# Performance work log

Hardware: AMD Instinct MI355X
Metric: run time of the kernel (lower is better)

The kernel has to match this reference:

```python
import jax, jax.numpy as jnp
import numpy as np

B, S, E = 2, 2048, 2048
H, KVH = 16, 4
D = E // H            # 128
N_REP = H // KVH      # 4


def setup_inputs() -> dict:
    key = jax.random.key(0)
    ks = jax.random.split(key, 5)
    x = jax.random.normal(ks[0], (B, S, E), dtype=jnp.float32)
    # kaiming-normal-ish linear weights, torch layout [out_features, in_features]
    wq_w = jax.random.normal(ks[1], (H * D, E), dtype=jnp.float32) * (2.0 / E) ** 0.5
    wk_w = jax.random.normal(ks[2], (KVH * D, E), dtype=jnp.float32) * (2.0 / E) ** 0.5
    wv_w = jax.random.normal(ks[3], (KVH * D, E), dtype=jnp.float32) * (2.0 / E) ** 0.5
    wo_w = jax.random.normal(ks[4], (E, E), dtype=jnp.float32) * (2.0 / E) ** 0.5
    # standard RoPE frequencies: theta = 10000
    inv_freq = 1.0 / (10000.0 ** (np.arange(0, D, 2, dtype=np.float32) / D))  # [D/2]
    t = np.arange(S, dtype=np.float32)
    ang = np.outer(t, inv_freq)  # [S, D/2]
    freqs_cos = jnp.asarray(np.cos(ang), dtype=jnp.float32)
    freqs_sin = jnp.asarray(np.sin(ang), dtype=jnp.float32)
    return {"x": x, "wq_w": wq_w, "wk_w": wk_w, "wv_w": wv_w, "wo_w": wo_w,
            "freqs_cos": freqs_cos, "freqs_sin": freqs_sin, "start_pos": 0}


def _rope(t, cos, sin):
    # t: [B, S, h, D]; cos/sin: [S, D/2] -> complex multiply on (even, odd) pairs
    tr = t.reshape(*t.shape[:-1], -1, 2)
    xr, xi = tr[..., 0], tr[..., 1]
    c = cos[None, :, None, :]
    s = sin[None, :, None, :]
    orr = xr * c - xi * s
    oi = xr * s + xi * c
    return jnp.stack([orr, oi], axis=-1).reshape(t.shape)


def reference(x, wq_w, wk_w, wv_w, wo_w, freqs_cos, freqs_sin, start_pos):
    b, s, e = x.shape
    q = jnp.einsum('bse,fe->bsf', x, wq_w).reshape(b, s, H, D)
    k = jnp.einsum('bse,fe->bsf', x, wk_w).reshape(b, s, KVH, D)
    v = jnp.einsum('bse,fe->bsf', x, wv_w).reshape(b, s, KVH, D)
    q = _rope(q, freqs_cos, freqs_sin)
    k = _rope(k, freqs_cos, freqs_sin)
    # faithful to torch .repeat(1,1,n_rep,1): TILE kv heads -> head h uses kv head h % KVH
    k = jnp.tile(k, (1, 1, N_REP, 1))  # [b, s, H, D]
    v = jnp.tile(v, (1, 1, N_REP, 1))
    q = q.transpose(0, 2, 1, 3)  # [b, H, s, D]
    k = k.transpose(0, 2, 1, 3)
    v = v.transpose(0, 2, 1, 3)
    scores = jnp.einsum('bhqd,bhkd->bhqk', q, k) * (1.0 / D ** 0.5)
    causal = jnp.tril(jnp.ones((s, s), dtype=bool))
    scores = jnp.where(causal[None, None], scores, -jnp.inf)
    attn = jax.nn.softmax(scores, axis=-1)
    out = jnp.einsum('bhqk,bhkd->bhqd', attn, v)
    out = out.transpose(0, 2, 1, 3).reshape(b, s, e)
    return jnp.einsum('bse,fe->bsf', out, wo_w)
```

## Files before the change

### kernel.cpp

```cpp
#include <hip/hip_runtime.h>
#include <hip/hip_bf16.h>

typedef unsigned short u16;
typedef unsigned int u32;
typedef short bf16x8 __attribute__((ext_vector_type(8)));
typedef float f32x4 __attribute__((ext_vector_type(4)));

#define MFMA_BF16 __builtin_amdgcn_mfma_f32_16x16x32_bf16

#define B_   2
#define S_   2048
#define E_   2048
#define H_   16
#define KVH_ 4
#define D_   128
#define M_   (B_ * S_)
#define NQKV 3072
#define SCALE_ 0.08838834764831845f

__device__ __forceinline__ float b2f(u16 u) {
    union { u32 i; float f; } x; x.i = ((u32)u) << 16; return x.f;
}
__device__ __forceinline__ u16 f2b(float f) {
    __hip_bfloat16 h = __float2bfloat16(f);
    return *reinterpret_cast<u16*>(&h);
}

__device__ __forceinline__ void async16(const u16* g, u16* l) {
    __builtin_amdgcn_global_load_lds(
        (const __attribute__((address_space(1))) void*)g,
        (__attribute__((address_space(3))) void*)l, 16, 0, 0);
}

__device__ __forceinline__ uint4 pack8(const float* p) {
    float4 a = *reinterpret_cast<const float4*>(p);
    float4 b = *reinterpret_cast<const float4*>(p + 4);
    union { uint4 v; u16 h[8]; } pk;
    pk.h[0] = f2b(a.x); pk.h[1] = f2b(a.y); pk.h[2] = f2b(a.z); pk.h[3] = f2b(a.w);
    pk.h[4] = f2b(b.x); pk.h[5] = f2b(b.y); pk.h[6] = f2b(b.z); pk.h[7] = f2b(b.w);
    return pk.v;
}

__global__ __launch_bounds__(256)
void conv4(const float* __restrict__ s0, u16* __restrict__ d0, int n0,
           const float* __restrict__ s1, u16* __restrict__ d1, int n1,
           const float* __restrict__ s2, u16* __restrict__ d2, int n2,
           const float* __restrict__ s3, u16* __restrict__ d3) {
    int bid = blockIdx.x;
    const float* s; u16* d; size_t base;
    if (bid < n0)                { s = s0; d = d0; base = (size_t)bid * 2048; }
    else if (bid < n0 + n1)      { s = s1; d = d1; base = (size_t)(bid - n0) * 2048; }
    else if (bid < n0 + n1 + n2) { s = s2; d = d2; base = (size_t)(bid - n0 - n1) * 2048; }
    else                         { s = s3; d = d3; base = (size_t)(bid - n0 - n1 - n2) * 2048; }
    size_t i = base + (size_t)threadIdx.x * 8;
    *reinterpret_cast<uint4*>(d + i) = pack8(s + i);
}

template <int BN>
__device__ __forceinline__ void gemm_core(const u16* __restrict__ Ag,
                                          const u16* __restrict__ Bg,
                                          u16* lds, int m0,
                                          f32x4 (&acc)[8][BN / 64]) {
    constexpr int NREP  = BN / 64;
    constexpr int BUFSZ = 16384 + BN * 64;
    constexpr int BJ    = BN / 128;
    const int tid = threadIdx.x, wave = tid >> 6, lane = tid & 63;
    const int l15 = lane & 15, quad = lane >> 4;
    const int wm = wave & 1, wn = wave >> 1;

    const f32x4 zero4 = {0.f, 0.f, 0.f, 0.f};
    #pragma unroll
    for (int i = 0; i < 8; ++i)
        #pragma unroll
        for (int j = 0; j < NREP; ++j) acc[i][j] = zero4;

    auto stageA = [&](int p, int kt, int kb) {
        #pragma unroll
        for (int j = 0; j < 2; ++j) {
            const int rb = wave * 2 + j;
            async16(Ag + (size_t)(m0 + rb * 16 + l15) * E_ + kt + kb * 32 + quad * 8,
                    &lds[p * BUFSZ + (((rb << 1) | kb) << 9)]);
        }
    };
    auto stageB = [&](int p, int kt, int kb) {
        #pragma unroll
        for (int j = 0; j < BJ; ++j) {
            const int rb = wave * BJ + j;
            async16(Bg + (size_t)(rb * 16 + l15) * E_ + kt + kb * 32 + quad * 8,
                    &lds[p * BUFSZ + 16384 + (((rb << 1) | kb) << 9)]);
        }
    };
    auto sync_keepN = [&]() {
        if constexpr (BN == 256) asm volatile("s_waitcnt vmcnt(4)" ::: "memory");
        else                     asm volatile("s_waitcnt vmcnt(3)" ::: "memory");
        __builtin_amdgcn_sched_barrier(0);
        __builtin_amdgcn_s_barrier();
        __builtin_amdgcn_sched_barrier(0);
    };
    auto sync_drain = [&]() {
        asm volatile("s_waitcnt vmcnt(0)" ::: "memory");
        __builtin_amdgcn_sched_barrier(0);
        __builtin_amdgcn_s_barrier();
        __builtin_amdgcn_sched_barrier(0);
    };

    auto half = [&](int p, int kb, bool stage, int ktn) {
        bf16x8 bfr[NREP];
        #pragma unroll
        for (int ni = 0; ni < NREP; ++ni)
            bfr[ni] = *reinterpret_cast<const bf16x8*>(
                &lds[p * BUFSZ + 16384 + ((((wn * NREP + ni) << 1) | kb) << 9) + lane * 8]);
        if (stage) stageA(p ^ 1, ktn, kb);
        bf16x8 af[4];
        #pragma unroll
        for (int i = 0; i < 4; ++i)
            af[i] = *reinterpret_cast<const bf16x8*>(
                &lds[p * BUFSZ + ((((wm * 8 + i) << 1) | kb) << 9) + lane * 8]);
        __builtin_amdgcn_s_setprio(1);
        #pragma unroll
        for (int mi = 0; mi < 4; ++mi)
            #pragma unroll
            for (int ni = 0; ni < NREP; ++ni)
                acc[mi][ni] = MFMA_BF16(af[mi], bfr[ni], acc[mi][ni], 0, 0, 0);
        __builtin_amdgcn_s_setprio(0);
        if (stage) stageB(p ^ 1, ktn, kb);
        #pragma unroll
        for (int i = 0; i < 4; ++i)
            af[i] = *reinterpret_cast<const bf16x8*>(
                &lds[p * BUFSZ + ((((wm * 8 + 4 + i) << 1) | kb) << 9) + lane * 8]);
        __builtin_amdgcn_s_setprio(1);
        #pragma unroll
        for (int mi = 0; mi < 4; ++mi)
            #pragma unroll
            for (int ni = 0; ni < NREP; ++ni)
                acc[4 + mi][ni] = MFMA_BF16(af[mi], bfr[ni], acc[4 + mi][ni], 0, 0, 0);
        __builtin_amdgcn_s_setprio(0);
    };

    stageA(0, 0, 0); stageB(0, 0, 0);
    stageA(0, 0, 1); stageB(0, 0, 1);
    sync_keepN();

    int p = 0;
    for (int kt = 0; kt < E_ - 64; kt += 64) {
        half(p, 0, true, kt + 64);
        sync_keepN();
        half(p, 1, true, kt + 64);
        sync_keepN();
        p ^= 1;
    }
    half(p, 0, false, 0);
    sync_drain();
    half(p, 1, false, 0);
}

__global__ __launch_bounds__(512, 2)
void qkv_rope_gemm(const u16* __restrict__ xb, const u16* __restrict__ wqb,
                   const u16* __restrict__ wkb, const u16* __restrict__ wvb,
                   const float* __restrict__ fc, const float* __restrict__ fs,
                   u16* __restrict__ Qr, u16* __restrict__ Kr,
                   u16* __restrict__ Vr) {
    __shared__ __align__(16) u16 lds[2 * (16384 + 256 * 64)];
    const int m0 = blockIdx.y * 256, n0 = blockIdx.x * 256;

    const u16* wsel;
    if (n0 < 2048)      wsel = wqb + (size_t)n0 * E_;
    else if (n0 < 2560) wsel = wkb + (size_t)(n0 - 2048) * E_;
    else                wsel = wvb + (size_t)(n0 - 2560) * E_;

    f32x4 acc[8][4];
    gemm_core<256>(xb, wsel, lds, m0, acc);

    const int tid = threadIdx.x, wave = tid >> 6, lane = tid & 63;
    const int l15 = lane & 15, quad = lane >> 4;
    const int wm = wave & 1, wn = wave >> 1;
    const int mb_ = m0 + wm * 128, nbase = n0 + wn * 64;
    #pragma unroll
    for (int mi = 0; mi < 8; ++mi)
        #pragma unroll
        for (int ni = 0; ni < 4; ++ni)
            #pragma unroll
            for (int r = 0; r < 4; ++r) {
                int m = mb_ + mi * 16 + quad * 4 + r;
                int n = nbase + ni * 16 + l15;
                int b = m >> 11, s = m & 2047;
                float v = acc[mi][ni][r];
                float other = __shfl_xor(v, 1);
                if (n < 2560) {
                    int d = n & 127;
                    int fi = s * 64 + (d >> 1);
                    float c  = fc[fi];
                    float sn = fs[fi];
                    v = (n & 1) ? (other * sn + v * c) : (v * c - other * sn);
                }
                if (n < 2048) {
                    Qr[((size_t)(b * H_ + (n >> 7)) * S_ + s) * D_ + (n & 127)] = f2b(v);
                } else if (n < 2560) {
                    int kh = (n - 2048) >> 7;
                    Kr[((size_t)(b * KVH_ + kh) * S_ + s) * D_ + (n & 127)] = f2b(v);
                } else {
                    int kh = (n - 2560) >> 7;
                    Vr[((size_t)(b * KVH_ + kh) * S_ + s) * D_ + (n & 127)] = f2b(v);
                }
            }
}

__global__ __launch_bounds__(256)
void transpose_v(const u16* __restrict__ Vr, u16* __restrict__ VrT) {
    __shared__ u16 t[64][72];
    const int tid = threadIdx.x;
    const int s0 = blockIdx.x * 64, d0 = blockIdx.y * 64, g = blockIdx.z;
    const u16* src = Vr + (size_t)g * S_ * D_;
    u16* dst = VrT + (size_t)g * D_ * S_;
    #pragma unroll
    for (int i = 0; i < 2; ++i) {
        int c = tid + i * 256;
        int r = c >> 3, cc = (c & 7) * 8;
        *reinterpret_cast<uint4*>(&t[r][cc]) =
            *reinterpret_cast<const uint4*>(src + (size_t)(s0 + r) * D_ + d0 + cc);
    }
    __syncthreads();
    #pragma unroll
    for (int i = 0; i < 2; ++i) {
        int c = tid + i * 256;
        int r = c >> 3, cc = (c & 7) * 8;
        u16 tmp[8];
        #pragma unroll
        for (int e = 0; e < 8; ++e) tmp[e] = t[cc + e][r];
        *reinterpret_cast<uint4*>(dst + (size_t)(d0 + r) * S_ + s0 + cc) =
            *reinterpret_cast<const uint4*>(tmp);
    }
}

__global__ __launch_bounds__(512, 4)
void flash2(const u16* __restrict__ Qr, const u16* __restrict__ Kr,
            const u16* __restrict__ VrT, u16* __restrict__ AO) {
    __shared__ __align__(16) u16 Ks[2][8192];
    __shared__ __align__(16) u16 Vs[2][8192];
    const int tid = threadIdx.x, wave = tid >> 6, lane = tid & 63;
    const int l15 = lane & 15, quad = lane >> 4;
    const int qt = gridDim.x - 1 - blockIdx.x;
    const int h = blockIdx.y, b = blockIdx.z;
    const int kvh = h & 3;
    const u16* Qb = Qr + (size_t)(b * H_ + h) * S_ * D_;
    const u16* Kb = Kr + (size_t)(b * KVH_ + kvh) * S_ * D_;
    const u16* Vb = VrT + (size_t)(b * KVH_ + kvh) * D_ * S_;
    const int q0 = qt * 128 + wave * 16;
    const int qg = q0 + l15;

    bf16x8 bq[4];
    #pragma unroll
    for (int kk = 0; kk < 4; ++kk)
        bq[kk] = *reinterpret_cast<const bf16x8*>(
            Qb + (size_t)qg * D_ + kk * 32 + quad * 8);

    f32x4 o[8];
    const f32x4 zero4 = {0.f, 0.f, 0.f, 0.f};
    #pragma unroll
    for (int i = 0; i < 8; ++i) o[i] = zero4;
    float m_i = -__builtin_inff(), l_i = 0.f;

    const int f0 = wave * 2, f1 = wave * 2 + 1;
    const u16* kp0 = Kb + (size_t)((f0 >> 2) * 16 + l15) * D_ + (f0 & 3) * 32 + quad * 8;
    const u16* kp1 = Kb + (size_t)((f1 >> 2) * 16 + l15) * D_ + (f1 & 3) * 32 + quad * 8;
    const u16* vp0 = Vb + (size_t)((f0 >> 1) * 16 + l15) * S_ + (f0 & 1) * 32 + quad * 8;
    const u16* vp1 = Vb + (size_t)((f1 >> 1) * 16 + l15) * S_ + (f1 & 1) * 32 + quad * 8;

    const int nt = 2 * qt + 2;
    async16(kp0, &Ks[0][f0 * 512]);
    async16(kp1, &Ks[0][f1 * 512]);
    async16(vp0, &Vs[0][f0 * 512]);
    async16(vp1, &Vs[0][f1 * 512]);

    int p = 0;
    for (int t = 0; t < nt; ++t) {
        __builtin_amdgcn_s_barrier();
        if (t + 1 < nt) {
            size_t ko = (size_t)(t + 1) * 64 * D_;
            size_t vo = (size_t)(t + 1) * 64;
            async16(kp0 + ko, &Ks[p ^ 1][f0 * 512]);
            async16(kp1 + ko, &Ks[p ^ 1][f1 * 512]);
            async16(vp0 + vo, &Vs[p ^ 1][f0 * 512]);
            async16(vp1 + vo, &Vs[p ^ 1][f1 * 512]);
            asm volatile("s_waitcnt vmcnt(4)" ::: "memory");
        } else {
            asm volatile("s_waitcnt vmcnt(0)" ::: "memory");
        }
        __builtin_amdgcn_sched_barrier(0);
        __builtin_amdgcn_s_barrier();
        __builtin_amdgcn_sched_barrier(0);

        const int kvbase = t * 64;
        if (q0 + 15 >= kvbase) {
            f32x4 st[4];
            #pragma unroll
            for (int kb = 0; kb < 4; ++kb) st[kb] = zero4;
            __builtin_amdgcn_s_setprio(1);
            #pragma unroll
            for (int kk = 0; kk < 4; ++kk)
                #pragma unroll
                for (int kb = 0; kb < 4; ++kb) {
                    bf16x8 ak = *reinterpret_cast<const bf16x8*>(
                        &Ks[p][(((kb << 2) | kk) << 9) + lane * 8]);
                    st[kb] = MFMA_BF16(ak, bq[kk], st[kb], 0, 0, 0);
                }
            __builtin_amdgcn_s_setprio(0);

            float mx = -__builtin_inff();
            if (kvbase + 63 > q0) {
                #pragma unroll
                for (int kb = 0; kb < 4; ++kb)
                    #pragma unroll
                    for (int r = 0; r < 4; ++r) {
                        float s = st[kb][r] * SCALE_;
                        if (kvbase + kb * 16 + quad * 4 + r > qg)
                            s = -__builtin_inff();
                        st[kb][r] = s;
                        mx = fmaxf(mx, s);
                    }
            } else {
                #pragma unroll
                for (int kb = 0; kb < 4; ++kb)
                    #pragma unroll
                    for (int r = 0; r < 4; ++r) {
                        float s = st[kb][r] * SCALE_;
                        st[kb][r] = s;
                        mx = fmaxf(mx, s);
                    }
            }
            mx = fmaxf(mx, __shfl_xor(mx, 16));
            mx = fmaxf(mx, __shfl_xor(mx, 32));
            const bool nodefer = !__all(mx - m_i <= 8.0f);
            float mnew = nodefer ? fmaxf(m_i, mx) : m_i;
            float a = __expf(m_i - mnew);
            float sum = 0.f;
            #pragma unroll
            for (int kb = 0; kb < 4; ++kb)
                #pragma unroll
                for (int r = 0; r < 4; ++r) {
                    float pv = __expf(st[kb][r] - mnew);
                    st[kb][r] = pv;
                    sum += pv;
                }
            sum += __shfl_xor(sum, 16);
            sum += __shfl_xor(sum, 32);
            l_i = l_i * a + sum;
            m_i = mnew;
            if (nodefer) {
                #pragma unroll
                for (int mi = 0; mi < 8; ++mi)
                    #pragma unroll
                    for (int r = 0; r < 4; ++r) o[mi][r] *= a;
            }

            #pragma unroll
            for (int kf = 0; kf < 2; ++kf) {
                u32 pk[4];
                #pragma unroll
                for (int r = 0; r < 4; ++r)
                    pk[r] = (u32)f2b(st[kf * 2 + 0][r]) |
                            ((u32)f2b(st[kf * 2 + 1][r]) << 16);
                bf16x8 bp;
                u16* bh = (u16*)&bp;
                #pragma unroll
                for (int j2 = 0; j2 < 8; ++j2) {
                    int src = ((quad & 1) * 2 + (j2 >> 2)) * 16 + l15;
                    u32 v = __shfl((int)pk[j2 & 3], src);
                    bh[j2] = (lane >= 32) ? (u16)(v >> 16) : (u16)v;
                }
                __builtin_amdgcn_s_setprio(1);
                #pragma unroll
                for (int mi = 0; mi < 8; ++mi) {
                    bf16x8 av = *reinterpret_cast<const bf16x8*>(
                        &Vs[p][(((mi << 1) | kf) << 9) + lane * 8]);
                    o[mi] = MFMA_BF16(av, bp, o[mi], 0, 0, 0);
                }
                __builtin_amdgcn_s_setprio(0);
            }
        }
        p ^= 1;
    }

    float inv = 1.0f / l_i;
    size_t base = ((size_t)(b * S_ + qg)) * E_ + h * D_;
    #pragma unroll
    for (int mi = 0; mi < 8; ++mi) {
        u16 w[4];
        #pragma unroll
        for (int r = 0; r < 4; ++r) w[r] = f2b(o[mi][r] * inv);
        *reinterpret_cast<uint2*>(AO + base + mi * 16 + quad * 4) =
            *reinterpret_cast<const uint2*>(w);
    }
}

__global__ __launch_bounds__(512, 2)
void out_proj_gemm(const u16* __restrict__ ao, const u16* __restrict__ wob,
                   float* __restrict__ out) {
    __shared__ __align__(16) u16 lds[2 * (16384 + 128 * 64)];
    const int m0 = blockIdx.y * 256, n0 = blockIdx.x * 128;

    f32x4 acc[8][2];
    gemm_core<128>(ao, wob + (size_t)n0 * E_, lds, m0, acc);

    const int tid = threadIdx.x, wave = tid >> 6, lane = tid & 63;
    const int l15 = lane & 15, quad = lane >> 4;
    const int wm = wave & 1, wn = wave >> 1;
    const int mb_ = m0 + wm * 128, nbase = n0 + wn * 32;
    #pragma unroll
    for (int mi = 0; mi < 8; ++mi)
        #pragma unroll
        for (int ni = 0; ni < 2; ++ni)
            #pragma unroll
            for (int r = 0; r < 4; ++r) {
                int m = mb_ + mi * 16 + quad * 4 + r;
                int n = nbase + ni * 16 + l15;
                out[(size_t)m * E_ + n] = acc[mi][ni][r];
            }
}

extern "C" void kernel_launch(void* const* d_in, const int* in_sizes, int n_in,
                              void* d_out, int out_size, void* d_ws, size_t ws_size,
                              hipStream_t stream) {
    const float* x  = (const float*)d_in[0];
    const float* wq = (const float*)d_in[1];
    const float* wk = (const float*)d_in[2];
    const float* wv = (const float*)d_in[3];
    const float* wo = (const float*)d_in[4];
    const float* fc = (const float*)d_in[5];
    const float* fs = (const float*)d_in[6];
    float* out = (float*)d_out;

    u16* wqb = (u16*)d_ws;
    u16* xb  = wqb + 4194304;
    u16* Qr  = wqb + 12582912;
    u16* Kr  = wqb + 20971520;
    u16* Vr  = wqb + 23068672;
    u16* VrT = wqb;
    u16* wob = wqb;
    u16* AO  = xb;
    u16* wkb = (u16*)d_out;
    u16* wvb = wkb + 1048576;

    conv4<<<7168, 256, 0, stream>>>(x, xb, 4096, wq, wqb, 2048,
                                    wk, wkb, 512, wv, wvb);
    qkv_rope_gemm<<<dim3(NQKV / 256, M_ / 256), 512, 0, stream>>>(
        xb, wqb, wkb, wvb, fc, fs, Qr, Kr, Vr);
    transpose_v<<<dim3(S_ / 64, D_ / 64, B_ * KVH_), 256, 0, stream>>>(Vr, VrT);
    flash2<<<dim3(S_ / 128, H_, B_), 512, 0, stream>>>(Qr, Kr, VrT, AO);
    conv4<<<2048, 256, 0, stream>>>(wo, wob, 2048, nullptr, nullptr, 0,
                                    nullptr, nullptr, 0, nullptr, nullptr);
    out_proj_gemm<<<dim3(E_ / 128, M_ / 256), 512, 0, stream>>>(AO, wob, out);
}
```

Before: 380.3 us.

## Split flash attention KV range across two wave groups per block

```diff
diff --git a/kernel.cpp b/kernel.cpp
--- a/kernel.cpp
+++ b/kernel.cpp
@@ -232,20 +232,23 @@
     }
 }
 
-__global__ __launch_bounds__(512, 4)
+__global__ __launch_bounds__(1024, 4)
 void flash2(const u16* __restrict__ Qr, const u16* __restrict__ Kr,
             const u16* __restrict__ VrT, u16* __restrict__ AO) {
-    __shared__ __align__(16) u16 Ks[2][8192];
-    __shared__ __align__(16) u16 Vs[2][8192];
+    __shared__ __align__(16) u16 Ks[2][2][8192];
+    __shared__ __align__(16) u16 Vs[2][2][8192];
     const int tid = threadIdx.x, wave = tid >> 6, lane = tid & 63;
+    const int grp = wave >> 3, gw = wave & 7;
     const int l15 = lane & 15, quad = lane >> 4;
-    const int qt = gridDim.x - 1 - blockIdx.x;
-    const int h = blockIdx.y, b = blockIdx.z;
+    const int lin = blockIdx.x;
+    const int qt  = 15 - (lin >> 5);
+    const int sub = lin & 31;
+    const int h = sub & 15, b = sub >> 4;
     const int kvh = h & 3;
     const u16* Qb = Qr + (size_t)(b * H_ + h) * S_ * D_;
     const u16* Kb = Kr + (size_t)(b * KVH_ + kvh) * S_ * D_;
     const u16* Vb = VrT + (size_t)(b * KVH_ + kvh) * D_ * S_;
-    const int q0 = qt * 128 + wave * 16;
+    const int q0 = qt * 128 + gw * 16;
     const int qg = q0 + l15;
 
     bf16x8 bq[4];
@@ -260,28 +263,33 @@
     for (int i = 0; i < 8; ++i) o[i] = zero4;
     float m_i = -__builtin_inff(), l_i = 0.f;
 
-    const int f0 = wave * 2, f1 = wave * 2 + 1;
-    const u16* kp0 = Kb + (size_t)((f0 >> 2) * 16 + l15) * D_ + (f0 & 3) * 32 + quad * 8;
-    const u16* kp1 = Kb + (size_t)((f1 >> 2) * 16 + l15) * D_ + (f1 & 3) * 32 + quad * 8;
-    const u16* vp0 = Vb + (size_t)((f0 >> 1) * 16 + l15) * S_ + (f0 & 1) * 32 + quad * 8;
-    const u16* vp1 = Vb + (size_t)((f1 >> 1) * 16 + l15) * S_ + (f1 & 1) * 32 + quad * 8;
-
-    const int nt = 2 * qt + 2;
-    async16(kp0, &Ks[0][f0 * 512]);
-    async16(kp1, &Ks[0][f1 * 512]);
-    async16(vp0, &Vs[0][f0 * 512]);
-    async16(vp1, &Vs[0][f1 * 512]);
+    const int nt = qt + 1;
+    const int tbase = grp ? nt : 0;
+    const int f0 = gw * 2, f1 = gw * 2 + 1;
+    const u16* kp0 = Kb + (size_t)tbase * 64 * D_ +
+        (size_t)((f0 >> 2) * 16 + l15) * D_ + (f0 & 3) * 32 + quad * 8;
+    const u16* kp1 = Kb + (size_t)tbase * 64 * D_ +
+        (size_t)((f1 >> 2) * 16 + l15) * D_ + (f1 & 3) * 32 + quad * 8;
+    const u16* vp0 = Vb + (size_t)tbase * 64 +
+        (size_t)((f0 >> 1) * 16 + l15) * S_ + (f0 & 1) * 32 + quad * 8;
+    const u16* vp1 = Vb + (size_t)tbase * 64 +
+        (size_t)((f1 >> 1) * 16 + l15) * S_ + (f1 & 1) * 32 + quad * 8;
+
+    async16(kp0, &Ks[grp][0][f0 * 512]);
+    async16(kp1, &Ks[grp][0][f1 * 512]);
+    async16(vp0, &Vs[grp][0][f0 * 512]);
+    async16(vp1, &Vs[grp][0][f1 * 512]);
 
     int p = 0;
-    for (int t = 0; t < nt; ++t) {
+    for (int i = 0; i < nt; ++i) {
         __builtin_amdgcn_s_barrier();
-        if (t + 1 < nt) {
-            size_t ko = (size_t)(t + 1) * 64 * D_;
-            size_t vo = (size_t)(t + 1) * 64;
-            async16(kp0 + ko, &Ks[p ^ 1][f0 * 512]);
-            async16(kp1 + ko, &Ks[p ^ 1][f1 * 512]);
-            async16(vp0 + vo, &Vs[p ^ 1][f0 * 512]);
-            async16(vp1 + vo, &Vs[p ^ 1][f1 * 512]);
+        if (i + 1 < nt) {
+            size_t ko = (size_t)(i + 1) * 64 * D_;
+            size_t vo = (size_t)(i + 1) * 64;
+            async16(kp0 + ko, &Ks[grp][p ^ 1][f0 * 512]);
+            async16(kp1 + ko, &Ks[grp][p ^ 1][f1 * 512]);
+            async16(vp0 + vo, &Vs[grp][p ^ 1][f0 * 512]);
+            async16(vp1 + vo, &Vs[grp][p ^ 1][f1 * 512]);
             asm volatile("s_waitcnt vmcnt(4)" ::: "memory");
         } else {
             asm volatile("s_waitcnt vmcnt(0)" ::: "memory");
@@ -290,7 +298,7 @@
         __builtin_amdgcn_s_barrier();
         __builtin_amdgcn_sched_barrier(0);
 
-        const int kvbase = t * 64;
+        const int kvbase = (tbase + i) * 64;
         if (q0 + 15 >= kvbase) {
             f32x4 st[4];
             #pragma unroll
@@ -301,7 +309,7 @@
                 #pragma unroll
                 for (int kb = 0; kb < 4; ++kb) {
                     bf16x8 ak = *reinterpret_cast<const bf16x8*>(
-                        &Ks[p][(((kb << 2) | kk) << 9) + lane * 8]);
+                        &Ks[grp][p][(((kb << 2) | kk) << 9) + lane * 8]);
                     st[kb] = MFMA_BF16(ak, bq[kk], st[kb], 0, 0, 0);
                 }
             __builtin_amdgcn_s_setprio(0);
@@ -372,7 +380,7 @@
                 #pragma unroll
                 for (int mi = 0; mi < 8; ++mi) {
                     bf16x8 av = *reinterpret_cast<const bf16x8*>(
-                        &Vs[p][(((mi << 1) | kf) << 9) + lane * 8]);
+                        &Vs[grp][p][(((mi << 1) | kf) << 9) + lane * 8]);
                     o[mi] = MFMA_BF16(av, bp, o[mi], 0, 0, 0);
                 }
                 __builtin_amdgcn_s_setprio(0);
@@ -381,15 +389,38 @@
         p ^= 1;
     }
 
-    float inv = 1.0f / l_i;
-    size_t base = ((size_t)(b * S_ + qg)) * E_ + h * D_;
-    #pragma unroll
-    for (int mi = 0; mi < 8; ++mi) {
-        u16 w[4];
-        #pragma unroll
-        for (int r = 0; r < 4; ++r) w[r] = f2b(o[mi][r] * inv);
-        *reinterpret_cast<uint2*>(AO + base + mi * 16 + quad * 4) =
-            *reinterpret_cast<const uint2*>(w);
+    float* shf = (float*)&Ks[0][0][0];
+    float* shm = (float*)&Vs[0][0][0];
+    __syncthreads();
+    if (grp == 1) {
+        #pragma unroll
+        for (int mi = 0; mi < 8; ++mi)
+            #pragma unroll
+            for (int r = 0; r < 4; ++r)
+                shf[((mi << 2) | r) * 512 + gw * 64 + lane] = o[mi][r];
+        shm[gw * 64 + lane] = m_i;
+        shm[512 + gw * 64 + lane] = l_i;
+    }
+    __syncthreads();
+    if (grp == 0) {
+        float m1 = shm[gw * 64 + lane];
+        float l1 = shm[512 + gw * 64 + lane];
+        float M  = fmaxf(m_i, m1);
+        float w0 = __expf(m_i - M), w1 = __expf(m1 - M);
+        float inv = 1.0f / (w0 * l_i + w1 * l1);
+        size_t base = ((size_t)(b * S_ + qg)) * E_ + h * D_;
+        #pragma unroll
+        for (int mi = 0; mi < 8; ++mi) {
+            u16 w[4];
+            #pragma unroll
+            for (int r = 0; r < 4; ++r) {
+                float ov = w0 * o[mi][r] +
+                           w1 * shf[((mi << 2) | r) * 512 + gw * 64 + lane];
+                w[r] = f2b(ov * inv);
+            }
+            *reinterpret_cast<uint2*>(AO + base + mi * 16 + quad * 4) =
+                *reinterpret_cast<const uint2*>(w);
+        }
     }
 }
 
@@ -446,7 +477,7 @@
     qkv_rope_gemm<<<dim3(NQKV / 256, M_ / 256), 512, 0, stream>>>(
         xb, wqb, wkb, wvb, fc, fs, Qr, Kr, Vr);
     transpose_v<<<dim3(S_ / 64, D_ / 64, B_ * KVH_), 256, 0, stream>>>(Vr, VrT);
-    flash2<<<dim3(S_ / 128, H_, B_), 512, 0, stream>>>(Qr, Kr, VrT, AO);
+    flash2<<<dim3(512), 1024, 0, stream>>>(Qr, Kr, VrT, AO);
     conv4<<<2048, 256, 0, stream>>>(wo, wob, 2048, nullptr, nullptr, 0,
                                     nullptr, nullptr, 0, nullptr, nullptr);
     out_proj_gemm<<<dim3(E_ / 128, M_ / 256), 512, 0, stream>>>(AO, wob, out);
```

Measured after the change: 348.5 us. 8.4% less time.
